# Optimization experiments

Measured on AMD Instinct MI355X. Metric: run time of the kernel, lower is better.

## Reference

```python
import jax, jax.numpy as jnp
import numpy as np

WS = 8            # window size (square)
HEADS = 16
HEAD_DIM = 32
DIM = 512
NEG_INF = float('-inf')


def _create_mask(ws, disp, upper_lower, left_right):
    size = ws * ws
    m = np.zeros((size, size), dtype=np.float32)
    d = disp
    if upper_lower:
        m[-d * ws:, :-d * ws] = NEG_INF
        m[:-d * ws, -d * ws:] = NEG_INF
    if left_right:
        m = m.reshape(ws, ws, ws, ws)
        m[:, -d:, :, :-d] = NEG_INF
        m[:, :-d, :, -d:] = NEG_INF
        m = m.reshape(size, size)
    return m


def _relative_indices(ws):
    coords = np.array([[x, y] for x in range(ws) for y in range(ws)])  # [ws^2, 2]
    dist = coords[None, :, :] - coords[:, None, :]                      # [ws^2, ws^2, 2]
    dist += ws - 1
    return dist.astype(np.int64)


_REL_IDX = _relative_indices(WS)                      # [64, 64, 2]
_UL_MASK = jnp.asarray(_create_mask(WS, WS // 2, True, False))   # [64, 64]
_LR_MASK = jnp.asarray(_create_mask(WS, WS // 2, False, True))   # [64, 64]


def setup_inputs() -> dict:
    key = jax.random.key(0)
    ks = jax.random.split(key, 5)
    b, n = 16, 64
    return {
        'x': jax.random.normal(ks[0], (b, n, n, DIM), dtype=jnp.float32),
        'w_qkv': jax.random.normal(ks[1], (3 * HEADS * HEAD_DIM, DIM), dtype=jnp.float32) * 0.02,
        'pos_embedding': jax.random.normal(ks[2], (2 * WS - 1, 2 * WS - 1), dtype=jnp.float32),
        'w_out': jax.random.normal(ks[3], (DIM, HEADS * HEAD_DIM), dtype=jnp.float32) * 0.02,
        'b_out': jax.random.normal(ks[4], (DIM,), dtype=jnp.float32) * 0.02,
    }


def reference(x, w_qkv, pos_embedding, w_out, b_out):
    disp = WS // 2
    scale = HEAD_DIM ** -0.5
    b, n_h, n_w, _ = x.shape
    nw_h, nw_w = n_h // WS, n_w // WS

    # cyclic shift (shifted=True)
    x = jnp.roll(x, shift=(-disp, -disp), axis=(1, 2))

    qkv = x @ w_qkv.T                                   # [b, n_h, n_w, 3*h*d]
    qkv = qkv.reshape(b, nw_h, WS, nw_w, WS, 3, HEADS, HEAD_DIM)
    # -> [3, b, heads, n_windows, window_tokens, head_dim]
    qkv = qkv.transpose(5, 0, 6, 1, 3, 2, 4, 7).reshape(
        3, b, HEADS, nw_h * nw_w, WS * WS, HEAD_DIM)
    q, k, v = qkv[0], qkv[1], qkv[2]

    dots = jnp.einsum('bhwid,bhwjd->bhwij', q, k) * scale
    # relative position bias
    dots = dots + pos_embedding[_REL_IDX[:, :, 0], _REL_IDX[:, :, 1]]
    # shift masks: last window-row and last window-column
    dots = dots.at[:, :, -nw_w:].add(_UL_MASK)
    dots = dots.at[:, :, nw_w - 1::nw_w].add(_LR_MASK)

    attn = jax.nn.softmax(dots, axis=-1)
    out = jnp.einsum('bhwij,bhwjd->bhwid', attn, v)     # [b,h,nw,ws^2,d]

    out = out.reshape(b, HEADS, nw_h, nw_w, WS, WS, HEAD_DIM)
    out = out.transpose(0, 2, 4, 3, 5, 1, 6).reshape(b, n_h, n_w, HEADS * HEAD_DIM)
    out = out @ w_out.T + b_out

    out = jnp.roll(out, shift=(disp, disp), axis=(1, 2))
    return out
```

## Files before the change

kernel.cpp:

```cpp
#include <hip/hip_runtime.h>
#include <hip/hip_bf16.h>
#include <stdint.h>

typedef __bf16 bf16;
typedef __attribute__((ext_vector_type(4))) float f32x4;
typedef __attribute__((ext_vector_type(8))) bf16 bf16x8;
typedef __attribute__((ext_vector_type(4))) bf16 bf16x4;

#define AS1 __attribute__((address_space(1)))
#define AS3 __attribute__((address_space(3)))

static __device__ __forceinline__ void gload_lds16(const bf16* g, bf16* l) {
  __builtin_amdgcn_global_load_lds((const AS1 void*)g, (AS3 void*)l, 16, 0, 0);
}

#define BAR __builtin_amdgcn_s_barrier()
#define SCHED0 __builtin_amdgcn_sched_barrier(0)
#define VMC_(n) asm volatile("s_waitcnt vmcnt(" #n ")" ::: "memory")
#define VMC(n) VMC_(n)
#define LGKM0 asm volatile("s_waitcnt lgkmcnt(0)" ::: "memory")

#define STAGE_A(gsrc, dst, kt_) do {                                          \
  _Pragma("unroll") for (int s_ = 0; s_ < 4; ++s_) {                          \
    int idx_ = s_ * 256 + tid;                                                \
    int r_ = idx_ >> 3, c_ = idx_ & 7;                                        \
    gload_lds16((gsrc) + (size_t)r_ * 512 + ((kt_) << 6) + ((c_ ^ (r_ & 7)) << 3), \
                (dst) + idx_ * 8);                                            \
  }                                                                           \
} while (0)

#define LOADB(ktq, NCOLX) do {                                                \
  const bf16* bp_ = Bptr + (size_t)(ktq) * ((size_t)(NCOLX) * 64);            \
  _Pragma("unroll") for (int cb_ = 0; cb_ < 4; ++cb_)                         \
  _Pragma("unroll") for (int ks_ = 0; ks_ < 2; ++ks_)                         \
    bfr[cb_][ks_] = *(const bf16x8*)(bp_ + cb_ * 128 + (size_t)ks_ * (NCOLX) * 32); \
} while (0)

#define KLOOP_BD(Ag, NCOLX)                                                   \
  f32x4 acc[4][4] = {};                                                       \
  bf16x8 af[4][2], bfr[4][2];                                                 \
  STAGE_A(Ag, SA0, 0);                                                        \
  LOADB(0, NCOLX);                                                            \
  VMC(8); BAR;                                                                \
  STAGE_A(Ag, SA1, 1);                                                        \
  _Pragma("unroll 2")                                                         \
  for (int kt = 0; kt < 8; ++kt) {                                            \
    bf16* Ap = (kt & 1) ? SA1 : SA0;                                          \
    _Pragma("unroll") for (int i_ = 0; i_ < 4; ++i_) {                        \
      int ra_ = wr + i_ * 16 + lr;                                            \
      _Pragma("unroll") for (int ks_ = 0; ks_ < 2; ++ks_)                     \
        af[i_][ks_] = *(const bf16x8*)(Ap + ra_ * 64 + (((ks_ * 4 + lg) ^ (ra_ & 7)) << 3)); \
    }                                                                         \
    LGKM0; SCHED0;                                                            \
    __builtin_amdgcn_s_setprio(1);                                            \
    _Pragma("unroll") for (int i_ = 0; i_ < 4; ++i_)                          \
    _Pragma("unroll") for (int j_ = 0; j_ < 4; ++j_)                          \
    _Pragma("unroll") for (int ks_ = 0; ks_ < 2; ++ks_)                       \
      acc[i_][j_] = __builtin_amdgcn_mfma_f32_16x16x32_bf16(                  \
          af[i_][ks_], bfr[j_][ks_], acc[i_][j_], 0, 0, 0);                   \
    __builtin_amdgcn_s_setprio(0);                                            \
    if (kt < 7) LOADB(kt + 1, NCOLX);                                         \
    if (kt < 7) { VMC(8); }                                                   \
    BAR;                                                                      \
    if (kt < 6) STAGE_A(Ag, Ap, kt + 2);                                      \
  }

__global__ __launch_bounds__(256) void prep_all(
    const float* __restrict__ x, const float* __restrict__ wqkv,
    const float* __restrict__ wout, const float* __restrict__ pos,
    bf16* __restrict__ xst, bf16* __restrict__ wqkv_bt,
    bf16* __restrict__ wout_bt, float* __restrict__ bias4) {
  const int blk = blockIdx.x, tid = threadIdx.x;
  if (blk < 1024) {
    int m = blk * 64 + (tid & 63);
    int w = tid >> 6;
    int b = m >> 12, win = (m >> 6) & 63, t = m & 63;
    int ip = ((win >> 3) << 3) + (t >> 3);
    int jp = ((win & 7) << 3) + (t & 7);
    int io = (ip + 4) & 63, jo = (jp + 4) & 63;
    const float* src = x + ((((size_t)(b << 6) + io) << 6) + jo) * 512;
    bf16* dst = xst + (size_t)m * 8;
    #pragma unroll
    for (int it = 0; it < 4; ++it) {
      int kb0 = w * 16 + it * 4;
      float4 v[8];
      #pragma unroll
      for (int q = 0; q < 8; ++q) v[q] = *(const float4*)(src + kb0 * 8 + q * 4);
      #pragma unroll
      for (int c = 0; c < 4; ++c) {
        bf16x8 o = { (bf16)v[2*c].x, (bf16)v[2*c].y, (bf16)v[2*c].z, (bf16)v[2*c].w,
                     (bf16)v[2*c+1].x, (bf16)v[2*c+1].y, (bf16)v[2*c+1].z, (bf16)v[2*c+1].w };
        *(bf16x8*)(dst + (size_t)(kb0 + c) * 524288) = o;
      }
    }
  } else if (blk < 1280) {
    int r = (blk - 1024) * 8 + (tid >> 5);
    int lane = tid & 31;
    const float* src;
    bf16* dstb;
    int ncol, col;
    float sc = 1.0f;
    if (r < 1536) {
      int part = r >> 9, h = (r >> 5) & 15, d = r & 31;
      src = wqkv + (size_t)r * 512; dstb = wqkv_bt; ncol = 1536;
      col = h * 96 + part * 32 + d;
      if (part == 0) sc = 0.17677669529663689f;
    } else {
      src = wout + (size_t)(r - 1536) * 512; dstb = wout_bt; ncol = 512; col = r - 1536;
    }
    #pragma unroll
    for (int kb = lane; kb < 64; kb += 32) {
      float4 v0 = *(const float4*)(src + kb * 8);
      float4 v1 = *(const float4*)(src + kb * 8 + 4);
      bf16x8 o = { (bf16)(v0.x * sc), (bf16)(v0.y * sc), (bf16)(v0.z * sc), (bf16)(v0.w * sc),
                   (bf16)(v1.x * sc), (bf16)(v1.y * sc), (bf16)(v1.z * sc), (bf16)(v1.w * sc) };
      *(bf16x8*)(dstb + ((size_t)kb * ncol + col) * 8) = o;
    }
  } else {
    int idx = (blk - 1280) * 256 + tid;
    int ty = idx >> 12, ij = idx & 4095;
    int i = ij >> 6, j = ij & 63;
    int rx = ((j >> 3) - (i >> 3)) + 7;
    int ry = ((j & 7) - (i & 7)) + 7;
    float v = pos[rx * 15 + ry];
    if ((ty & 1) && (((i ^ j) >> 5) & 1)) v = -1e30f;
    if ((ty & 2) && (((i ^ j) >> 2) & 1)) v = -1e30f;
    bias4[idx] = v;
  }
}

#define LOADAF(dst, ktq) do {                                                 \
  _Pragma("unroll") for (int i_ = 0; i_ < 2; ++i_)                            \
  _Pragma("unroll") for (int ks_ = 0; ks_ < 2; ++ks_)                         \
    dst[i_][ks_] = *(const bf16x8*)(Aptr + ((size_t)((ktq) * 8 + ks_ * 4 + lg)) * 524288 + i_ * 128); \
} while (0)

#define LOADB_H(set, ktq, hf) do {                                            \
  const bf16* bp_ = Bptr + (size_t)(ktq) * 98304 + (hf) * 384;                \
  _Pragma("unroll") for (int cb_ = 0; cb_ < 3; ++cb_)                         \
  _Pragma("unroll") for (int ks_ = 0; ks_ < 2; ++ks_)                         \
    set[cb_][ks_] = *(const bf16x8*)(bp_ + cb_ * 128 + ks_ * 49152);          \
} while (0)

#define MM3(afs, bs, j0)                                                      \
  _Pragma("unroll") for (int i_ = 0; i_ < 2; ++i_)                            \
  _Pragma("unroll") for (int jj_ = 0; jj_ < 3; ++jj_)                         \
  _Pragma("unroll") for (int ks_ = 0; ks_ < 2; ++ks_)                         \
    acc[i_][(j0) + jj_] = __builtin_amdgcn_mfma_f32_16x16x32_bf16(            \
        afs[i_][ks_], bs[jj_][ks_], acc[i_][(j0) + jj_], 0, 0, 0);

#define KTS(CUR, NXT, KT_, V2) do {                                           \
  VMC(6); SCHED0;                                                             \
  __builtin_amdgcn_s_setprio(1); MM3(CUR, bfrX, 0);                           \
  __builtin_amdgcn_s_setprio(0);                                              \
  if ((KT_) < 7) { LOADAF(NXT, (KT_) + 1); LOADB_H(bfrX, (KT_) + 1, 0); }     \
  VMC(V2); SCHED0;                                                            \
  __builtin_amdgcn_s_setprio(1); MM3(CUR, bfrY, 3);                           \
  __builtin_amdgcn_s_setprio(0);                                              \
  if ((KT_) < 7) LOADB_H(bfrY, (KT_) + 1, 1);                                 \
} while (0)

__global__ __launch_bounds__(256, 3) void qkv_attn(
    const bf16* __restrict__ xst, const bf16* __restrict__ wb2,
    const float* __restrict__ bias4, bf16* __restrict__ ao) {
  __shared__ bf16 smb[12288];

  const int tid = threadIdx.x, wave = tid >> 6, lane = tid & 63;
  const int ww = wave >> 1, rh = wave & 1;
  const int lr = lane & 15, lg = lane >> 4;

  int bid = blockIdx.x;
  bid = (bid & 7) * 1024 + (bid >> 3);
  const int mt = bid >> 4, h = bid & 15;

  const bf16* Aptr = xst + ((size_t)(mt * 128 + ww * 64 + rh * 32 + lr)) * 8;
  const bf16* Bptr = wb2 + (((size_t)lg * 1536) + h * 96 + lr) * 8;

  f32x4 acc[2][6] = {};
  bf16x8 afA[2][2], afB[2][2], bfrX[3][2], bfrY[3][2];

  LOADAF(afA, 0); LOADB_H(bfrX, 0, 0); LOADB_H(bfrY, 0, 1);
  KTS(afA, afB, 0, 10);
  KTS(afB, afA, 1, 10);
  KTS(afA, afB, 2, 10);
  KTS(afB, afA, 3, 10);
  KTS(afA, afB, 4, 10);
  KTS(afB, afA, 5, 10);
  KTS(afA, afB, 6, 10);
  KTS(afB, afA, 7, 0);

  bf16* Eu = smb + ww * 6144;
  bf16* Ev = Eu + 4096;
  #pragma unroll
  for (int i = 0; i < 2; ++i)
    #pragma unroll
    for (int r = 0; r < 4; ++r) {
      int row = rh * 32 + i * 16 + (lg << 2) + r;
      #pragma unroll
      for (int j = 0; j < 4; ++j) {
        int c = j * 16 + lr;
        Eu[row * 64 + (c ^ ((row & 7) << 3))] = (bf16)acc[i][j][r];
      }
      #pragma unroll
      for (int j = 4; j < 6; ++j) {
        int cv = (j - 4) * 16 + lr;
        Ev[cv * 64 + (row ^ ((cv & 7) << 3))] = (bf16)acc[i][j][r];
      }
    }
  LGKM0; BAR;

  bf16x8 qf[2], kf[4];
  #pragma unroll
  for (int i = 0; i < 2; ++i) {
    int ra = rh * 32 + i * 16 + lr;
    qf[i] = *(const bf16x8*)(Eu + ra * 64 + ((lg << 3) ^ ((ra & 7) << 3)));
  }
  #pragma unroll
  for (int j = 0; j < 4; ++j) {
    int rb = j * 16 + lr;
    kf[j] = *(const bf16x8*)(Eu + rb * 64 + ((32 + (lg << 3)) ^ ((rb & 7) << 3)));
  }
  f32x4 s[2][4] = {};
  #pragma unroll
  for (int i = 0; i < 2; ++i)
    #pragma unroll
    for (int j = 0; j < 4; ++j)
      s[i][j] = __builtin_amdgcn_mfma_f32_16x16x32_bf16(qf[i], kf[j], s[i][j], 0, 0, 0);

  const int gw = mt * 2 + ww;
  const int win = gw & 63;
  const int ty = ((win >= 56) ? 1 : 0) | (((win & 7) == 7) ? 2 : 0);
  const float* bt = bias4 + ty * 4096;
  #pragma unroll
  for (int i = 0; i < 2; ++i)
    #pragma unroll
    for (int r = 0; r < 4; ++r) {
      int grow = rh * 32 + i * 16 + (lg << 2) + r;
      #pragma unroll
      for (int j = 0; j < 4; ++j)
        s[i][j][r] += bt[grow * 64 + j * 16 + lr];
    }
  #pragma unroll
  for (int i = 0; i < 2; ++i)
    #pragma unroll
    for (int r = 0; r < 4; ++r) {
      float mx = fmaxf(fmaxf(s[i][0][r], s[i][1][r]), fmaxf(s[i][2][r], s[i][3][r]));
      mx = fmaxf(mx, __shfl_xor(mx, 1));
      mx = fmaxf(mx, __shfl_xor(mx, 2));
      mx = fmaxf(mx, __shfl_xor(mx, 4));
      mx = fmaxf(mx, __shfl_xor(mx, 8));
      float sum = 0.f;
      #pragma unroll
      for (int j = 0; j < 4; ++j) { s[i][j][r] = __expf(s[i][j][r] - mx); sum += s[i][j][r]; }
      sum += __shfl_xor(sum, 1);
      sum += __shfl_xor(sum, 2);
      sum += __shfl_xor(sum, 4);
      sum += __shfl_xor(sum, 8);
      float inv = 1.0f / sum;
      #pragma unroll
      for (int j = 0; j < 4; ++j) s[i][j][r] *= inv;
    }
  BAR;
  #pragma unroll
  for (int i = 0; i < 2; ++i)
    #pragma unroll
    for (int r = 0; r < 4; ++r) {
      int row = rh * 32 + i * 16 + (lg << 2) + r;
      #pragma unroll
      for (int j = 0; j < 4; ++j) {
        int c = j * 16 + lr;
        Eu[row * 64 + (c ^ ((row & 7) << 3))] = (bf16)s[i][j][r];
      }
    }
  LGKM0; SCHED0;
  bf16x8 vf[2][2];
  #pragma unroll
  for (int kk = 0; kk < 2; ++kk)
    #pragma unroll
    for (int nj = 0; nj < 2; ++nj) {
      int dv = nj * 16 + lr;
      vf[kk][nj] = *(const bf16x8*)(Ev + dv * 64 + ((kk * 32 + (lg << 3)) ^ ((dv & 7) << 3)));
    }
  f32x4 o[2][2] = {};
  #pragma unroll
  for (int kk = 0; kk < 2; ++kk)
    #pragma unroll
    for (int mi = 0; mi < 2; ++mi) {
      int ra = rh * 32 + mi * 16 + lr;
      bf16x8 pa = *(const bf16x8*)(Eu + ra * 64 + ((kk * 32 + (lg << 3)) ^ ((ra & 7) << 3)));
      #pragma unroll
      for (int nj = 0; nj < 2; ++nj)
        o[mi][nj] = __builtin_amdgcn_mfma_f32_16x16x32_bf16(pa, vf[kk][nj], o[mi][nj], 0, 0, 0);
    }
  bf16* dst = ao + ((size_t)(mt * 128 + ww * 64)) * 512 + h * 32;
  #pragma unroll
  for (int mi = 0; mi < 2; ++mi)
    #pragma unroll
    for (int r = 0; r < 4; ++r) {
      int t = rh * 32 + mi * 16 + (lg << 2) + r;
      #pragma unroll
      for (int nj = 0; nj < 2; ++nj)
        dst[(size_t)t * 512 + nj * 16 + lr] = (bf16)o[mi][nj][r];
    }
}

__global__ __launch_bounds__(256, 3) void gemm_out(
    const bf16* __restrict__ ao, const bf16* __restrict__ wob,
    const float* __restrict__ bout, float* __restrict__ out) {
  __shared__ bf16 SA[2][8192];
  bf16* SA0 = SA[0]; bf16* SA1 = SA[1];

  const int tid = threadIdx.x, wave = tid >> 6, lane = tid & 63;
  int bid = blockIdx.x;
  bid = (bid & 7) * 256 + (bid >> 3);
  const int mt = bid >> 2, nt = bid & 3;
  const bf16* Ag = ao + ((size_t)mt * 128) * 512;
  const int wr = (wave >> 1) << 6, wc = (wave & 1) << 6;
  const int lr = lane & 15, lg = lane >> 4;
  const bf16* Bptr = wob + (((size_t)lg * 512) + nt * 128 + wc + lr) * 8;

  KLOOP_BD(Ag, 512)

  float bv[4];
  #pragma unroll
  for (int j = 0; j < 4; ++j) bv[j] = bout[nt * 128 + wc + j * 16 + lr];
  #pragma unroll
  for (int i = 0; i < 4; ++i)
    #pragma unroll
    for (int r = 0; r < 4; ++r) {
      int m = (mt << 7) + wr + i * 16 + (lg << 2) + r;
      int b = m >> 12, win = (m >> 6) & 63, t = m & 63;
      int ip = ((win >> 3) << 3) + (t >> 3);
      int jp = ((win & 7) << 3) + (t & 7);
      int io = (ip + 4) & 63, jo = (jp + 4) & 63;
      float* orow = out + ((((size_t)(b << 6) + io) << 6) + jo) * 512 + nt * 128 + wc;
      #pragma unroll
      for (int j = 0; j < 4; ++j)
        orow[j * 16 + lr] = acc[i][j][r] + bv[j];
    }
}

extern "C" void kernel_launch(void* const* d_in, const int* in_sizes, int n_in,
                              void* d_out, int out_size, void* d_ws, size_t ws_size,
                              hipStream_t stream) {
  const float* x    = (const float*)d_in[0];
  const float* wqkv = (const float*)d_in[1];
  const float* pos  = (const float*)d_in[2];
  const float* wout = (const float*)d_in[3];
  const float* bout = (const float*)d_in[4];
  float* out = (float*)d_out;

  char* ws = (char*)d_ws;
  bf16* xst     = (bf16*)(ws);
  bf16* ao      = (bf16*)(ws + 67108864);
  bf16* wqkv_bt = (bf16*)(ws + 268435456);
  bf16* wout_bt = (bf16*)(ws + 270008320);
  float* bias4  = (float*)(ws + 270532608);

  prep_all<<<dim3(1344), dim3(256), 0, stream>>>(x, wqkv, wout, pos,
                                                 xst, wqkv_bt, wout_bt, bias4);
  qkv_attn<<<dim3(8192), dim3(256), 0, stream>>>(xst, wqkv_bt, bias4, ao);
  gemm_out<<<dim3(2048), dim3(256), 0, stream>>>(ao, wout_bt, bout, out);
}
```

Before: 260.2 us.

## Stage QKV weight tiles into LDS with double-buffered async loads

The weight-prep kernel now writes the QKV weights in a per-head, per-k-tile layout with an XOR swizzle. The QKV GEMM stages each k-tile of weights into double-buffered LDS using global_load_lds and reads the B fragments from LDS, where each wave previously loaded them from global memory itself. This shares one weight load across the four waves of the block and cuts redundant global traffic. The cost is a block barrier per k-step and reuse of the shared buffer that the attention epilogue also writes to.

```diff
diff --git a/kernel.cpp b/kernel.cpp
--- a/kernel.cpp
+++ b/kernel.cpp
@@ -96,25 +96,31 @@
   } else if (blk < 1280) {
     int r = (blk - 1024) * 8 + (tid >> 5);
     int lane = tid & 31;
-    const float* src;
-    bf16* dstb;
-    int ncol, col;
-    float sc = 1.0f;
     if (r < 1536) {
       int part = r >> 9, h = (r >> 5) & 15, d = r & 31;
-      src = wqkv + (size_t)r * 512; dstb = wqkv_bt; ncol = 1536;
-      col = h * 96 + part * 32 + d;
-      if (part == 0) sc = 0.17677669529663689f;
+      int col = part * 32 + d;
+      float sc = (part == 0) ? 0.17677669529663689f : 1.0f;
+      const float* src = wqkv + (size_t)r * 512;
+      #pragma unroll
+      for (int kb = lane; kb < 64; kb += 32) {
+        int kt = kb >> 3, ch = kb & 7;
+        float4 v0 = *(const float4*)(src + kb * 8);
+        float4 v1 = *(const float4*)(src + kb * 8 + 4);
+        bf16x8 o = { (bf16)(v0.x * sc), (bf16)(v0.y * sc), (bf16)(v0.z * sc), (bf16)(v0.w * sc),
+                     (bf16)(v1.x * sc), (bf16)(v1.y * sc), (bf16)(v1.z * sc), (bf16)(v1.w * sc) };
+        *(bf16x8*)(wqkv_bt + (size_t)(h * 8 + kt) * 6144 + col * 64 + ((ch ^ (col & 7)) << 3)) = o;
+      }
     } else {
-      src = wout + (size_t)(r - 1536) * 512; dstb = wout_bt; ncol = 512; col = r - 1536;
-    }
-    #pragma unroll
-    for (int kb = lane; kb < 64; kb += 32) {
-      float4 v0 = *(const float4*)(src + kb * 8);
-      float4 v1 = *(const float4*)(src + kb * 8 + 4);
-      bf16x8 o = { (bf16)(v0.x * sc), (bf16)(v0.y * sc), (bf16)(v0.z * sc), (bf16)(v0.w * sc),
-                   (bf16)(v1.x * sc), (bf16)(v1.y * sc), (bf16)(v1.z * sc), (bf16)(v1.w * sc) };
-      *(bf16x8*)(dstb + ((size_t)kb * ncol + col) * 8) = o;
+      int r2 = r - 1536;
+      const float* src = wout + (size_t)r2 * 512;
+      #pragma unroll
+      for (int kb = lane; kb < 64; kb += 32) {
+        float4 v0 = *(const float4*)(src + kb * 8);
+        float4 v1 = *(const float4*)(src + kb * 8 + 4);
+        bf16x8 o = { (bf16)v0.x, (bf16)v0.y, (bf16)v0.z, (bf16)v0.w,
+                     (bf16)v1.x, (bf16)v1.y, (bf16)v1.z, (bf16)v1.w };
+        *(bf16x8*)(wout_bt + ((size_t)kb * 512 + r2) * 8) = o;
+      }
     }
   } else {
     int idx = (blk - 1280) * 256 + tid;
@@ -135,29 +141,34 @@
     dst[i_][ks_] = *(const bf16x8*)(Aptr + ((size_t)((ktq) * 8 + ks_ * 4 + lg)) * 524288 + i_ * 128); \
 } while (0)
 
-#define LOADB_H(set, ktq, hf) do {                                            \
-  const bf16* bp_ = Bptr + (size_t)(ktq) * 98304 + (hf) * 384;                \
-  _Pragma("unroll") for (int cb_ = 0; cb_ < 3; ++cb_)                         \
+#define STAGE_B(dstbuf, ktq) do {                                             \
+  const bf16* src_ = Bh + (size_t)(ktq) * 6144;                               \
+  _Pragma("unroll") for (int s_ = 0; s_ < 3; ++s_) {                          \
+    int idx_ = s_ * 256 + tid;                                                \
+    gload_lds16(src_ + idx_ * 8, (dstbuf) + idx_ * 8);                        \
+  }                                                                           \
+} while (0)
+
+#define KTB(CUR, NXT, KT_) do {                                               \
+  const bf16* Bp_ = smb + ((KT_) & 1) * 6144;                                 \
+  _Pragma("unroll") for (int cb_ = 0; cb_ < 6; ++cb_)                         \
+  _Pragma("unroll") for (int ks_ = 0; ks_ < 2; ++ks_) {                       \
+    int col_ = cb_ * 16 + lr;                                                 \
+    bfr[cb_][ks_] = *(const bf16x8*)(Bp_ + col_ * 64 + (((ks_ * 4 + lg) ^ (col_ & 7)) << 3)); \
+  }                                                                           \
+  if ((KT_) < 7) LOADAF(NXT, (KT_) + 1);                                      \
+  if ((KT_) < 7) { VMC(7); } else { VMC(0); }                                 \
+  LGKM0; SCHED0;                                                              \
+  __builtin_amdgcn_s_setprio(1);                                              \
+  _Pragma("unroll") for (int i_ = 0; i_ < 2; ++i_)                            \
+  _Pragma("unroll") for (int j_ = 0; j_ < 6; ++j_)                            \
   _Pragma("unroll") for (int ks_ = 0; ks_ < 2; ++ks_)                         \
-    set[cb_][ks_] = *(const bf16x8*)(bp_ + cb_ * 128 + ks_ * 49152);          \
-} while (0)
-
-#define MM3(afs, bs, j0)                                                      \
-  _Pragma("unroll") for (int i_ = 0; i_ < 2; ++i_)                            \
-  _Pragma("unroll") for (int jj_ = 0; jj_ < 3; ++jj_)                         \
-  _Pragma("unroll") for (int ks_ = 0; ks_ < 2; ++ks_)                         \
-    acc[i_][(j0) + jj_] = __builtin_amdgcn_mfma_f32_16x16x32_bf16(            \
-        afs[i_][ks_], bs[jj_][ks_], acc[i_][(j0) + jj_], 0, 0, 0);
-
-#define KTS(CUR, NXT, KT_, V2) do {                                           \
-  VMC(6); SCHED0;                                                             \
-  __builtin_amdgcn_s_setprio(1); MM3(CUR, bfrX, 0);                           \
+    acc[i_][j_] = __builtin_amdgcn_mfma_f32_16x16x32_bf16(                    \
+        CUR[i_][ks_], bfr[j_][ks_], acc[i_][j_], 0, 0, 0);                    \
   __builtin_amdgcn_s_setprio(0);                                              \
-  if ((KT_) < 7) { LOADAF(NXT, (KT_) + 1); LOADB_H(bfrX, (KT_) + 1, 0); }     \
-  VMC(V2); SCHED0;                                                            \
-  __builtin_amdgcn_s_setprio(1); MM3(CUR, bfrY, 3);                           \
-  __builtin_amdgcn_s_setprio(0);                                              \
-  if ((KT_) < 7) LOADB_H(bfrY, (KT_) + 1, 1);                                 \
+  if ((KT_) < 7) { VMC(4); }                                                  \
+  BAR;                                                                        \
+  if ((KT_) < 6) STAGE_B(smb + ((KT_) & 1) * 6144, (KT_) + 2);                \
 } while (0)
 
 __global__ __launch_bounds__(256, 3) void qkv_attn(
@@ -174,20 +185,24 @@
   const int mt = bid >> 4, h = bid & 15;
 
   const bf16* Aptr = xst + ((size_t)(mt * 128 + ww * 64 + rh * 32 + lr)) * 8;
-  const bf16* Bptr = wb2 + (((size_t)lg * 1536) + h * 96 + lr) * 8;
+  const bf16* Bh = wb2 + (size_t)h * 49152;
 
   f32x4 acc[2][6] = {};
-  bf16x8 afA[2][2], afB[2][2], bfrX[3][2], bfrY[3][2];
-
-  LOADAF(afA, 0); LOADB_H(bfrX, 0, 0); LOADB_H(bfrY, 0, 1);
-  KTS(afA, afB, 0, 10);
-  KTS(afB, afA, 1, 10);
-  KTS(afA, afB, 2, 10);
-  KTS(afB, afA, 3, 10);
-  KTS(afA, afB, 4, 10);
-  KTS(afB, afA, 5, 10);
-  KTS(afA, afB, 6, 10);
-  KTS(afB, afA, 7, 0);
+  bf16x8 afA[2][2], afB[2][2], bfr[6][2];
+
+  STAGE_B(smb, 0);
+  LOADAF(afA, 0);
+  VMC(4); BAR;
+  STAGE_B(smb + 6144, 1);
+
+  KTB(afA, afB, 0);
+  KTB(afB, afA, 1);
+  KTB(afA, afB, 2);
+  KTB(afB, afA, 3);
+  KTB(afA, afB, 4);
+  KTB(afB, afA, 5);
+  KTB(afA, afB, 6);
+  KTB(afB, afA, 7);
 
   bf16* Eu = smb + ww * 6144;
   bf16* Ev = Eu + 4096;
```

Result: faster. 246.8 us (median of 3 runs) (-5.2%).
